# Kernel optimization log

Hardware: AMD Instinct MI355X
Metric: run time of the kernel (lower is better)

The kernel has to match this reference:

```python
import jax, jax.numpy as jnp
import numpy as np

IN_FEATURES = 1024
OUT_FEATURES = 1024
GRID_SIZE = 5
SPLINE_ORDER = 3
N_BASIS = GRID_SIZE + SPLINE_ORDER  # 8, matches spline_weight last dim
N_GRID = GRID_SIZE + 2 * SPLINE_ORDER + 1  # 12 knots -> Cox-de-Boor yields N_BASIS bases


def b_spline(x, grid):
    # x: [B, I] -> bases: [B, I, N_BASIS]
    x = x[..., None]
    bases = ((x >= grid[:-1]) & (x < grid[1:])).astype(x.dtype)
    for k in range(1, SPLINE_ORDER + 1):
        left = (x - grid[: -k - 1]) / (grid[k:-1] - grid[: -k - 1] + 1e-8)
        right = (grid[k + 1:] - x) / (grid[k + 1:] - grid[1:-k] + 1e-8)
        bases = left * bases[..., :-1] + right * bases[..., 1:]
    return bases


def setup_inputs() -> dict:
    key = jax.random.key(0)
    k1, k2, k3 = jax.random.split(key, 3)
    x = jax.random.uniform(k1, (4096, IN_FEATURES), dtype=jnp.float32) * 2.0 - 1.0
    # kaiming_uniform_(a=sqrt(5)) on [out,in]: bound = 1/sqrt(in)
    bound = 1.0 / np.sqrt(IN_FEATURES)
    base_weight = jax.random.uniform(k2, (OUT_FEATURES, IN_FEATURES), dtype=jnp.float32,
                                     minval=-bound, maxval=bound)
    spline_weight = 0.1 * jax.random.normal(k3, (OUT_FEATURES, IN_FEATURES, N_BASIS), dtype=jnp.float32)
    grid = jnp.linspace(-1.0, 1.0, N_GRID, dtype=jnp.float32)
    return {"x": x, "base_weight": base_weight, "spline_weight": spline_weight, "grid": grid}


def reference(x, base_weight, spline_weight, grid):
    base_output = jax.nn.silu(x) @ base_weight.T  # [B, O]
    spline_basis = b_spline(x, grid)              # [B, I, Q]
    spline_output = jnp.einsum('biq,oiq->bo', spline_basis, spline_weight)
    return base_output + spline_output
```

## Files before the change

kernel.cpp:

```cpp
#include <hip/hip_runtime.h>
#include <hip/hip_bf16.h>

#define IN_F 1024
#define OUT_F 1024
#define QP 9
#define KDIM (IN_F * QP)
#define BM 256
#define BN 256
#define BK 64
#define TILE_SH (BM * BK)

typedef __attribute__((ext_vector_type(8)))  short short8;
typedef __attribute__((ext_vector_type(16))) float floatx16;
typedef __attribute__((ext_vector_type(8)))  unsigned short ushort8v;

__device__ __forceinline__ unsigned short f2bf(float f) {
    union { float f; unsigned u; } v; v.f = f;
    return (unsigned short)((v.u + 0x7FFF + ((v.u >> 16) & 1)) >> 16);
}
__device__ __forceinline__ float bf2f(unsigned short h) {
    union { unsigned u; float f; } v; v.u = ((unsigned)h) << 16;
    return v.f;
}

__global__ __launch_bounds__(256) void pack_kernel(const float* __restrict__ x,
                                                   const float* __restrict__ bw,
                                                   const float* __restrict__ sw,
                                                   __hip_bfloat16* __restrict__ A,
                                                   __hip_bfloat16* __restrict__ W, int Bm) {
    const int nb_a = (Bm * IN_F / 8) / 256;
    if ((int)blockIdx.x < nb_a) {
        int t  = blockIdx.x * 256 + threadIdx.x;
        int b  = t >> 7;
        int i0 = (t & 127) * 8;
        const float4* xr = (const float4*)(x + (size_t)b * IN_F + i0);
        float4 x0 = xr[0], x1 = xr[1];
        float xv[8] = {x0.x, x0.y, x0.z, x0.w, x1.x, x1.y, x1.z, x1.w};
        ushort8v ov[9];
#pragma unroll
        for (int e = 0; e < 8; ++e) {
            float v  = xv[e];
            float u  = (v + 1.0f) * 5.5f;
            float fj = floorf(u);
            int   j  = (int)fj;
            float tt = u - fj;
            float t2 = tt * tt, t3 = t2 * tt;
            float omt = 1.0f - tt;
            float w0 = omt * omt * omt * (1.0f / 6.0f);
            float w1 = (3.0f * t3 - 6.0f * t2 + 4.0f) * (1.0f / 6.0f);
            float w2 = (-3.0f * t3 + 3.0f * t2 + 3.0f * tt + 1.0f) * (1.0f/6.0f);
            float w3 = t3 * (1.0f / 6.0f);
            ov[0][e] = f2bf(v * __builtin_amdgcn_rcpf(1.0f + __expf(-v)));
#pragma unroll
            for (int q = 0; q < 8; ++q) {
                int d = j - q;
                float bv = (d == 3) ? w0 : (d == 2) ? w1 : (d == 1) ? w2 : (d == 0) ? w3 : 0.0f;
                ov[1 + q][e] = f2bf(bv);
            }
        }
        unsigned short* dst = (unsigned short*)A + (size_t)b * KDIM + i0;
#pragma unroll
        for (int s = 0; s < QP; ++s)
            *(ushort8v*)(dst + (size_t)s * IN_F) = ov[s];
    } else {
        int t = ((int)blockIdx.x - nb_a) * 256 + threadIdx.x;
        unsigned short* dst = (unsigned short*)W + (size_t)(t >> 10) * KDIM + (t & 1023);
        dst[0] = f2bf(bw[t]);
        const float4* s4 = (const float4*)(sw + (size_t)t * 8);
        float4 lo = s4[0], hi = s4[1];
        dst[1 * IN_F] = f2bf(lo.x); dst[2 * IN_F] = f2bf(lo.y);
        dst[3 * IN_F] = f2bf(lo.z); dst[4 * IN_F] = f2bf(lo.w);
        dst[5 * IN_F] = f2bf(hi.x); dst[6 * IN_F] = f2bf(hi.y);
        dst[7 * IN_F] = f2bf(hi.z); dst[8 * IN_F] = f2bf(hi.w);
    }
}

#define GLD(src, dst) __builtin_amdgcn_global_load_lds( \
        (const __attribute__((address_space(1))) void*)(src), \
        (__attribute__((address_space(3))) void*)(dst), 16, 0, 0)

__global__ __launch_bounds__(512, 2) void gemm_splitk(const __hip_bfloat16* __restrict__ A,
                                                      const __hip_bfloat16* __restrict__ W,
                                                      unsigned short* __restrict__ P,
                                                      int Bm, int splitk, int kslice) {
    __shared__ __align__(16) short sA[2][TILE_SH];
    __shared__ __align__(16) short sB[2][TILE_SH];
    const int tid  = threadIdx.x;
    const int lane = tid & 63;
    const int wave = tid >> 6;
    const int r32  = lane & 31;
    const int half = lane >> 5;
    const int wm   = wave >> 2;
    const int wn   = wave & 3;

    const int b   = (int)blockIdx.x;
    const int xcd = b & 7, ii = b >> 3;
    const int pp  = xcd * (splitk >> 1) + (ii >> 4);
    const int xt  = pp & 3, zt = pp >> 2, yt = ii & 15;
    const int m0 = yt * BM, n0 = xt * BN, kb = zt * kslice;
    const int NT = kslice / BK;

    const short* Ag = (const short*)A + (size_t)m0 * KDIM + kb;
    const short* Wg = (const short*)W + (size_t)n0 * KDIM + kb;

    const short* pA[4]; const short* pB[4]; int ldst[4];
#pragma unroll
    for (int u = 0; u < 4; ++u) {
        int c  = u * 512 + tid;
        int gs = ((c & 7) ^ ((c >> 3) & 7)) * 8;
        pA[u] = Ag + (size_t)(c >> 3) * KDIM + gs;
        pB[u] = Wg + (size_t)(c >> 3) * KDIM + gs;
        ldst[u] = c * 8;
    }

    const int sw7 = r32 & 7;
    int offA[4][4], offB[2][4];
#pragma unroll
    for (int mi = 0; mi < 4; ++mi) {
        int row = wm * 128 + mi * 32 + r32;
#pragma unroll
        for (int kc = 0; kc < 4; ++kc)
            offA[mi][kc] = row * BK + (((kc * 2 + half) ^ sw7) * 8);
    }
#pragma unroll
    for (int ni = 0; ni < 2; ++ni) {
        int row = wn * 64 + ni * 32 + r32;
#pragma unroll
        for (int kc = 0; kc < 4; ++kc)
            offB[ni][kc] = row * BK + (((kc * 2 + half) ^ sw7) * 8);
    }

    floatx16 acc[4][2] = {};

#define STAGE(bi, koff) do { \
        _Pragma("unroll") \
        for (int u = 0; u < 4; ++u) { \
            GLD(pA[u] + (koff), &sA[bi][ldst[u]]); \
            GLD(pB[u] + (koff), &sB[bi][ldst[u]]); \
        } \
    } while (0)

    STAGE(0, 0);

    for (int t = 0; t < NT; ++t) {
        asm volatile("s_waitcnt vmcnt(0)" ::: "memory");
        __builtin_amdgcn_s_barrier();

        const int nb = (t + 1 == NT) ? 0 : t + 1;
        STAGE((t + 1) & 1, nb * BK);

        const short* sAb = &sA[t & 1][0];
        const short* sBb = &sB[t & 1][0];

        __builtin_amdgcn_s_setprio(1);
#pragma unroll
        for (int kc = 0; kc < 4; ++kc) {
            short8 aF[4], bF[2];
#pragma unroll
            for (int mi = 0; mi < 4; ++mi) aF[mi] = *(const short8*)(sAb + offA[mi][kc]);
#pragma unroll
            for (int ni = 0; ni < 2; ++ni) bF[ni] = *(const short8*)(sBb + offB[ni][kc]);
#pragma unroll
            for (int mi = 0; mi < 4; ++mi)
#pragma unroll
                for (int ni = 0; ni < 2; ++ni)
                    acc[mi][ni] = __builtin_amdgcn_mfma_f32_32x32x16_bf16(
                        aF[mi], bF[ni], acc[mi][ni], 0, 0, 0);
        }
        __builtin_amdgcn_s_setprio(0);
    }
#undef STAGE
    asm volatile("s_waitcnt vmcnt(0)" ::: "memory");

    unsigned short* Pz = P + (size_t)zt * Bm * OUT_F;
#pragma unroll
    for (int mi = 0; mi < 4; ++mi)
#pragma unroll
        for (int ni = 0; ni < 2; ++ni)
#pragma unroll
            for (int r = 0; r < 16; ++r) {
                int row = (r & 3) + 8 * (r >> 2) + 4 * half;
                int gm  = m0 + wm * 128 + mi * 32 + row;
                Pz[(size_t)gm * OUT_F + n0 + wn * 64 + ni * 32 + r32] = f2bf(acc[mi][ni][r]);
            }
}

__global__ __launch_bounds__(256) void reduce_kernel(const unsigned short* __restrict__ P,
                                                     float* __restrict__ C, int n, int s) {
    int t  = blockIdx.x * 256 + threadIdx.x;
    int i0 = t * 8;
    float o[8] = {0.f, 0.f, 0.f, 0.f, 0.f, 0.f, 0.f, 0.f};
    for (int j = 0; j < s; ++j) {
        ushort8v a = *(const ushort8v*)(P + (size_t)j * n + i0);
#pragma unroll
        for (int e = 0; e < 8; ++e) o[e] += bf2f(a[e]);
    }
    float4 o0, o1;
    o0.x = o[0]; o0.y = o[1]; o0.z = o[2]; o0.w = o[3];
    o1.x = o[4]; o1.y = o[5]; o1.z = o[6]; o1.w = o[7];
    *(float4*)(C + i0)     = o0;
    *(float4*)(C + i0 + 4) = o1;
}

__global__ __launch_bounds__(256) void fallback_kernel(const float* __restrict__ x,
                                                       const float* __restrict__ bw,
                                                       const float* __restrict__ sw,
                                                       const float* __restrict__ grid,
                                                       float* __restrict__ out, int Bm) {
    __shared__ float sv[256][QP + 1];
    int b = blockIdx.y;
    int o = blockIdx.x * 256 + threadIdx.x;
    float acc = 0.f;
    for (int ic = 0; ic < IN_F; ic += 256) {
        int i = ic + threadIdx.x;
        float v = x[(size_t)b * IN_F + i];
        float g[12];
        for (int j = 0; j < 12; ++j) g[j] = grid[j];
        float bb[11];
        for (int j = 0; j < 11; ++j) bb[j] = (v >= g[j] && v < g[j + 1]) ? 1.f : 0.f;
        for (int k = 1; k <= 3; ++k)
            for (int j = 0; j < 11 - k; ++j)
                bb[j] = (v - g[j]) / (g[j + k] - g[j] + 1e-8f) * bb[j]
                      + (g[j + k + 1] - v) / (g[j + k + 1] - g[j + 1] + 1e-8f) * bb[j + 1];
        __syncthreads();
        sv[threadIdx.x][0] = v / (1.f + __expf(-v));
        for (int q = 0; q < 8; ++q) sv[threadIdx.x][1 + q] = bb[q];
        __syncthreads();
        for (int ii = 0; ii < 256; ++ii) {
            int i2 = ic + ii;
            acc += sv[ii][0] * bw[(size_t)o * IN_F + i2];
            const float* swp = sw + ((size_t)o * IN_F + i2) * 8;
            for (int q = 0; q < 8; ++q) acc += sv[ii][1 + q] * swp[q];
        }
    }
    out[(size_t)b * OUT_F + o] = acc;
}

extern "C" void kernel_launch(void* const* d_in, const int* in_sizes, int n_in,
                              void* d_out, int out_size, void* d_ws, size_t ws_size,
                              hipStream_t stream) {
    const float* x    = (const float*)d_in[0];
    const float* bw   = (const float*)d_in[1];
    const float* sw   = (const float*)d_in[2];
    const float* grid = (const float*)d_in[3];
    float* out = (float*)d_out;

    const int Bm = in_sizes[0] / IN_F;
    const size_t a_bytes = (size_t)Bm * KDIM * sizeof(__hip_bfloat16);
    const size_t w_bytes = (size_t)OUT_F * KDIM * sizeof(__hip_bfloat16);

    int splitk = 4;
    size_t p_bytes = (size_t)splitk * Bm * OUT_F * sizeof(unsigned short);
    if (ws_size < a_bytes + w_bytes + p_bytes) {
        splitk = 2;
        p_bytes = (size_t)splitk * Bm * OUT_F * sizeof(unsigned short);
    }

    if (ws_size >= a_bytes + w_bytes + p_bytes && Bm == 4096) {
        __hip_bfloat16* Apk = (__hip_bfloat16*)d_ws;
        __hip_bfloat16* Wpk = (__hip_bfloat16*)((char*)d_ws + a_bytes);
        unsigned short* P = (unsigned short*)((char*)d_ws + a_bytes + w_bytes);
        const int nb_a = (Bm * IN_F / 8) / 256;
        const int nb_w = (OUT_F * IN_F) / 256;
        pack_kernel<<<nb_a + nb_w, 256, 0, stream>>>(x, bw, sw, Apk, Wpk, Bm);
        gemm_splitk<<<(Bm / BM) * (OUT_F / BN) * splitk, 512, 0, stream>>>(
            Apk, Wpk, P, Bm, splitk, KDIM / splitk);
        reduce_kernel<<<Bm * OUT_F / 2048, 256, 0, stream>>>(P, out, Bm * OUT_F, splitk);
    } else {
        fallback_kernel<<<dim3(OUT_F / 256, Bm), 256, 0, stream>>>(x, bw, sw, grid, out, Bm);
    }
}
```

Measured before the change: 197.5 us.

## Split K-tile into halves and interleave fine-grained staging with MFMA phases

Stores each K tile in LDS as two 32-wide halves with a new XOR swizzle. The main loop becomes eight phases per two K-tiles, and each phase issues a slice of the next tile's global-to-LDS loads between its fragment reads and its MFMAs. Waits drop from vmcnt(0) to partial vmcnt(4), so loads overlap compute rather than stalling once per tile. The cost is two barriers per phase instead of one per tile, and the loop assumes an even tile count.

```diff
diff --git a/kernel.cpp b/kernel.cpp
--- a/kernel.cpp
+++ b/kernel.cpp
@@ -8,7 +8,7 @@
 #define BM 256
 #define BN 256
 #define BK 64
-#define TILE_SH (BM * BK)
+#define KH_SH 8192
 
 typedef __attribute__((ext_vector_type(8)))  short short8;
 typedef __attribute__((ext_vector_type(16))) float floatx16;
@@ -79,12 +79,16 @@
         (const __attribute__((address_space(1))) void*)(src), \
         (__attribute__((address_space(3))) void*)(dst), 16, 0, 0)
 
+#define VM4 asm volatile("s_waitcnt vmcnt(4)" ::: "memory")
+#define VM0 asm volatile("s_waitcnt vmcnt(0)" ::: "memory")
+#define NOPW ((void)0)
+
 __global__ __launch_bounds__(512, 2) void gemm_splitk(const __hip_bfloat16* __restrict__ A,
                                                       const __hip_bfloat16* __restrict__ W,
                                                       unsigned short* __restrict__ P,
                                                       int Bm, int splitk, int kslice) {
-    __shared__ __align__(16) short sA[2][TILE_SH];
-    __shared__ __align__(16) short sB[2][TILE_SH];
+    __shared__ __align__(16) short sA[2][2 * KH_SH];
+    __shared__ __align__(16) short sB[2][2 * KH_SH];
     const int tid  = threadIdx.x;
     const int lane = tid & 63;
     const int wave = tid >> 6;
@@ -99,78 +103,87 @@
     const int xt  = pp & 3, zt = pp >> 2, yt = ii & 15;
     const int m0 = yt * BM, n0 = xt * BN, kb = zt * kslice;
     const int NT = kslice / BK;
+    const int NI = NT >> 1;
 
     const short* Ag = (const short*)A + (size_t)m0 * KDIM + kb;
     const short* Wg = (const short*)W + (size_t)n0 * KDIM + kb;
 
-    const short* pA[4]; const short* pB[4]; int ldst[4];
-#pragma unroll
-    for (int u = 0; u < 4; ++u) {
-        int c  = u * 512 + tid;
-        int gs = ((c & 7) ^ ((c >> 3) & 7)) * 8;
-        pA[u] = Ag + (size_t)(c >> 3) * KDIM + gs;
-        pB[u] = Wg + (size_t)(c >> 3) * KDIM + gs;
-        ldst[u] = c * 8;
-    }
-
-    const int sw7 = r32 & 7;
+    const int rc0 = tid >> 2, rc1 = rc0 + 128;
+    const int gw0 = (((tid & 3) ^ ((tid >> 3) & 3)) * 8);
+    const int ld0 = tid * 8, ld1 = ld0 + 4096;
+
+#define STG(S, Base, bi, Kh, k0) do { \
+        GLD(Base + (size_t)rc0 * KDIM + (k0) + (Kh) * 32 + gw0, &S[bi][(Kh) * KH_SH + ld0]); \
+        GLD(Base + (size_t)rc1 * KDIM + (k0) + (Kh) * 32 + gw0, &S[bi][(Kh) * KH_SH + ld1]); \
+    } while (0)
+
+    const int s2 = (r32 >> 1) & 3;
     int offA[4][4], offB[2][4];
 #pragma unroll
     for (int mi = 0; mi < 4; ++mi) {
         int row = wm * 128 + mi * 32 + r32;
 #pragma unroll
         for (int kc = 0; kc < 4; ++kc)
-            offA[mi][kc] = row * BK + (((kc * 2 + half) ^ sw7) * 8);
+            offA[mi][kc] = (kc >> 1) * KH_SH + row * 32 + ((((kc & 1) * 2 + half) ^ s2) * 8);
     }
 #pragma unroll
     for (int ni = 0; ni < 2; ++ni) {
         int row = wn * 64 + ni * 32 + r32;
 #pragma unroll
         for (int kc = 0; kc < 4; ++kc)
-            offB[ni][kc] = row * BK + (((kc * 2 + half) ^ sw7) * 8);
+            offB[ni][kc] = (kc >> 1) * KH_SH + row * 32 + ((((kc & 1) * 2 + half) ^ s2) * 8);
     }
 
     floatx16 acc[4][2] = {};
 
-#define STAGE(bi, koff) do { \
+#define PHASE(pb, kc, DO_STAGE, DO_WAIT) do { \
+        short8 aF[4], bF[2]; \
         _Pragma("unroll") \
-        for (int u = 0; u < 4; ++u) { \
-            GLD(pA[u] + (koff), &sA[bi][ldst[u]]); \
-            GLD(pB[u] + (koff), &sB[bi][ldst[u]]); \
-        } \
+        for (int mi = 0; mi < 4; ++mi) aF[mi] = *(const short8*)&sA[pb][offA[mi][kc]]; \
+        _Pragma("unroll") \
+        for (int ni = 0; ni < 2; ++ni) bF[ni] = *(const short8*)&sB[pb][offB[ni][kc]]; \
+        DO_STAGE; \
+        __builtin_amdgcn_s_barrier(); \
+        __builtin_amdgcn_s_setprio(1); \
+        _Pragma("unroll") \
+        for (int mi = 0; mi < 4; ++mi) \
+            _Pragma("unroll") \
+            for (int ni = 0; ni < 2; ++ni) \
+                acc[mi][ni] = __builtin_amdgcn_mfma_f32_32x32x16_bf16( \
+                    aF[mi], bF[ni], acc[mi][ni], 0, 0, 0); \
+        __builtin_amdgcn_s_setprio(0); \
+        DO_WAIT; \
+        __builtin_amdgcn_s_barrier(); \
     } while (0)
 
-    STAGE(0, 0);
-
-    for (int t = 0; t < NT; ++t) {
-        asm volatile("s_waitcnt vmcnt(0)" ::: "memory");
-        __builtin_amdgcn_s_barrier();
-
-        const int nb = (t + 1 == NT) ? 0 : t + 1;
-        STAGE((t + 1) & 1, nb * BK);
-
-        const short* sAb = &sA[t & 1][0];
-        const short* sBb = &sB[t & 1][0];
-
-        __builtin_amdgcn_s_setprio(1);
-#pragma unroll
-        for (int kc = 0; kc < 4; ++kc) {
-            short8 aF[4], bF[2];
-#pragma unroll
-            for (int mi = 0; mi < 4; ++mi) aF[mi] = *(const short8*)(sAb + offA[mi][kc]);
-#pragma unroll
-            for (int ni = 0; ni < 2; ++ni) bF[ni] = *(const short8*)(sBb + offB[ni][kc]);
-#pragma unroll
-            for (int mi = 0; mi < 4; ++mi)
-#pragma unroll
-                for (int ni = 0; ni < 2; ++ni)
-                    acc[mi][ni] = __builtin_amdgcn_mfma_f32_32x32x16_bf16(
-                        aF[mi], bF[ni], acc[mi][ni], 0, 0, 0);
+    STG(sA, Ag, 0, 0, 0);
+    STG(sB, Wg, 0, 0, 0);
+    STG(sA, Ag, 0, 1, 0);
+    STG(sB, Wg, 0, 1, 0);
+    VM4;
+    __builtin_amdgcn_s_barrier();
+
+    for (int it = 0; it < NI; ++it) {
+        const int k1 = (2 * it + 1) * BK;
+        const int k2 = (2 * it + 2) * BK;
+        PHASE(0, 0, STG(sA, Ag, 1, 0, k1), NOPW);
+        PHASE(0, 1, STG(sB, Wg, 1, 0, k1), VM4);
+        PHASE(0, 2, STG(sA, Ag, 1, 1, k1), NOPW);
+        PHASE(0, 3, STG(sB, Wg, 1, 1, k1), VM4);
+        if (it + 1 < NI) {
+            PHASE(1, 0, STG(sA, Ag, 0, 0, k2), NOPW);
+            PHASE(1, 1, STG(sB, Wg, 0, 0, k2), VM4);
+            PHASE(1, 2, STG(sA, Ag, 0, 1, k2), NOPW);
+            PHASE(1, 3, STG(sB, Wg, 0, 1, k2), VM4);
+        } else {
+            PHASE(1, 0, NOPW, NOPW);
+            PHASE(1, 1, NOPW, VM0);
+            PHASE(1, 2, NOPW, NOPW);
+            PHASE(1, 3, NOPW, NOPW);
         }
-        __builtin_amdgcn_s_setprio(0);
-    }
-#undef STAGE
-    asm volatile("s_waitcnt vmcnt(0)" ::: "memory");
+    }
+#undef PHASE
+#undef STG
 
     unsigned short* Pz = P + (size_t)zt * Bm * OUT_F;
 #pragma unroll
```

Result: slower. 294.5 us (+49.1%).

## Fuse split-K reduction into GEMM via per-tile atomic arrival counter

Applied to the files above, without the earlier changes.

Drops the separate reduce kernel. Each GEMM block writes its bf16 partial tile, bumps a per-output-tile atomic counter, and the last of the four split-K blocks to arrive sums the partials and writes the fp32 output. The pack kernel zeroes the counters. This saves one kernel launch and a full pass over the partial buffer by a separate grid, at the cost of fences, an atomic, and tail work done only by the last-arriving blocks. Split-K is now fixed at 4, so the fallback to split 2 when workspace is small is gone.

```diff
diff --git a/kernel.cpp b/kernel.cpp
--- a/kernel.cpp
+++ b/kernel.cpp
@@ -8,6 +8,7 @@
 #define BM 256
 #define BN 256
 #define BK 64
+#define SPLITK 4
 #define TILE_SH (BM * BK)
 
 typedef __attribute__((ext_vector_type(8)))  short short8;
@@ -27,7 +28,9 @@
                                                    const float* __restrict__ bw,
                                                    const float* __restrict__ sw,
                                                    __hip_bfloat16* __restrict__ A,
-                                                   __hip_bfloat16* __restrict__ W, int Bm) {
+                                                   __hip_bfloat16* __restrict__ W,
+                                                   int* __restrict__ cnt, int Bm) {
+    if (blockIdx.x == 0 && threadIdx.x < 64) cnt[threadIdx.x] = 0;
     const int nb_a = (Bm * IN_F / 8) / 256;
     if ((int)blockIdx.x < nb_a) {
         int t  = blockIdx.x * 256 + threadIdx.x;
@@ -82,9 +85,11 @@
 __global__ __launch_bounds__(512, 2) void gemm_splitk(const __hip_bfloat16* __restrict__ A,
                                                       const __hip_bfloat16* __restrict__ W,
                                                       unsigned short* __restrict__ P,
-                                                      int Bm, int splitk, int kslice) {
+                                                      float* __restrict__ out,
+                                                      int* __restrict__ cnt, int Bm) {
     __shared__ __align__(16) short sA[2][TILE_SH];
     __shared__ __align__(16) short sB[2][TILE_SH];
+    __shared__ int s_old;
     const int tid  = threadIdx.x;
     const int lane = tid & 63;
     const int wave = tid >> 6;
@@ -93,9 +98,10 @@
     const int wm   = wave >> 2;
     const int wn   = wave & 3;
 
+    const int kslice = KDIM / SPLITK;
     const int b   = (int)blockIdx.x;
     const int xcd = b & 7, ii = b >> 3;
-    const int pp  = xcd * (splitk >> 1) + (ii >> 4);
+    const int pp  = xcd * 2 + (ii >> 4);
     const int xt  = pp & 3, zt = pp >> 2, yt = ii & 15;
     const int m0 = yt * BM, n0 = xt * BN, kb = zt * kslice;
     const int NT = kslice / BK;
@@ -172,7 +178,8 @@
 #undef STAGE
     asm volatile("s_waitcnt vmcnt(0)" ::: "memory");
 
-    unsigned short* Pz = P + (size_t)zt * Bm * OUT_F;
+    const size_t bmout = (size_t)Bm * OUT_F;
+    unsigned short* Pz = P + (size_t)zt * bmout;
 #pragma unroll
     for (int mi = 0; mi < 4; ++mi)
 #pragma unroll
@@ -183,23 +190,36 @@
                 int gm  = m0 + wm * 128 + mi * 32 + row;
                 Pz[(size_t)gm * OUT_F + n0 + wn * 64 + ni * 32 + r32] = f2bf(acc[mi][ni][r]);
             }
-}
-
-__global__ __launch_bounds__(256) void reduce_kernel(const unsigned short* __restrict__ P,
-                                                     float* __restrict__ C, int n, int s) {
-    int t  = blockIdx.x * 256 + threadIdx.x;
-    int i0 = t * 8;
-    float o[8] = {0.f, 0.f, 0.f, 0.f, 0.f, 0.f, 0.f, 0.f};
-    for (int j = 0; j < s; ++j) {
-        ushort8v a = *(const ushort8v*)(P + (size_t)j * n + i0);
-#pragma unroll
-        for (int e = 0; e < 8; ++e) o[e] += bf2f(a[e]);
-    }
-    float4 o0, o1;
-    o0.x = o[0]; o0.y = o[1]; o0.z = o[2]; o0.w = o[3];
-    o1.x = o[4]; o1.y = o[5]; o1.z = o[6]; o1.w = o[7];
-    *(float4*)(C + i0)     = o0;
-    *(float4*)(C + i0 + 4) = o1;
+
+    __syncthreads();
+    __threadfence();
+    if (tid == 0)
+        s_old = __hip_atomic_fetch_add(&cnt[yt * 4 + xt], 1,
+                                       __ATOMIC_ACQ_REL, __HIP_MEMORY_SCOPE_AGENT);
+    __syncthreads();
+    if (s_old == 3) {
+        __threadfence();
+        const size_t base = (size_t)m0 * OUT_F + n0;
+#pragma unroll 2
+        for (int it2 = 0; it2 < 16; ++it2) {
+            int idx  = it2 * 512 + tid;
+            int row  = idx >> 5;
+            int colc = idx & 31;
+            size_t off = base + (size_t)row * OUT_F + colc * 8;
+            float o[8] = {0.f, 0.f, 0.f, 0.f, 0.f, 0.f, 0.f, 0.f};
+#pragma unroll
+            for (int z = 0; z < 4; ++z) {
+                ushort8v a8 = *(const ushort8v*)(P + (size_t)z * bmout + off);
+#pragma unroll
+                for (int e = 0; e < 8; ++e) o[e] += bf2f(a8[e]);
+            }
+            float4 o0, o1;
+            o0.x = o[0]; o0.y = o[1]; o0.z = o[2]; o0.w = o[3];
+            o1.x = o[4]; o1.y = o[5]; o1.z = o[6]; o1.w = o[7];
+            *(float4*)(out + off)     = o0;
+            *(float4*)(out + off + 4) = o1;
+        }
+    }
 }
 
 __global__ __launch_bounds__(256) void fallback_kernel(const float* __restrict__ x,
@@ -248,24 +268,19 @@
     const int Bm = in_sizes[0] / IN_F;
     const size_t a_bytes = (size_t)Bm * KDIM * sizeof(__hip_bfloat16);
     const size_t w_bytes = (size_t)OUT_F * KDIM * sizeof(__hip_bfloat16);
-
-    int splitk = 4;
-    size_t p_bytes = (size_t)splitk * Bm * OUT_F * sizeof(unsigned short);
-    if (ws_size < a_bytes + w_bytes + p_bytes) {
-        splitk = 2;
-        p_bytes = (size_t)splitk * Bm * OUT_F * sizeof(unsigned short);
-    }
-
-    if (ws_size >= a_bytes + w_bytes + p_bytes && Bm == 4096) {
+    const size_t p_bytes = (size_t)SPLITK * Bm * OUT_F * sizeof(unsigned short);
+    const size_t c_bytes = 256;
+
+    if (ws_size >= a_bytes + w_bytes + p_bytes + c_bytes && Bm == 4096) {
         __hip_bfloat16* Apk = (__hip_bfloat16*)d_ws;
         __hip_bfloat16* Wpk = (__hip_bfloat16*)((char*)d_ws + a_bytes);
         unsigned short* P = (unsigned short*)((char*)d_ws + a_bytes + w_bytes);
+        int* cnt = (int*)((char*)d_ws + a_bytes + w_bytes + p_bytes);
         const int nb_a = (Bm * IN_F / 8) / 256;
         const int nb_w = (OUT_F * IN_F) / 256;
-        pack_kernel<<<nb_a + nb_w, 256, 0, stream>>>(x, bw, sw, Apk, Wpk, Bm);
-        gemm_splitk<<<(Bm / BM) * (OUT_F / BN) * splitk, 512, 0, stream>>>(
-            Apk, Wpk, P, Bm, splitk, KDIM / splitk);
-        reduce_kernel<<<Bm * OUT_F / 2048, 256, 0, stream>>>(P, out, Bm * OUT_F, splitk);
+        pack_kernel<<<nb_a + nb_w, 256, 0, stream>>>(x, bw, sw, Apk, Wpk, cnt, Bm);
+        gemm_splitk<<<(Bm / BM) * (OUT_F / BN) * SPLITK, 512, 0, stream>>>(
+            Apk, Wpk, P, out, cnt, Bm);
     } else {
         fallback_kernel<<<dim3(OUT_F / 256, Bm), 256, 0, stream>>>(x, bw, sw, grid, out, Bm);
     }
```

Result: slower. 288.0 us (+45.8%).

## Shrink GEMM tile to 256x128 single-buffered for higher occupancy

Applied to the files above, without the earlier changes.

Reduces the split-K GEMM output tile from 256x256 to 256x128 and drops LDS double buffering in favour of a load-wait-compute-barrier loop. The aim is to fit more blocks per CU (launch bounds 6), so other resident blocks hide global-load latency. Split-K is fixed at compile time and the LDS swizzle is changed for the new tile shape. In exchange, each block reuses less data per loaded tile, global traffic for A doubles, and there is no longer any prefetch overlap within a block.

```diff
diff --git a/kernel.cpp b/kernel.cpp
--- a/kernel.cpp
+++ b/kernel.cpp
@@ -6,9 +6,11 @@
 #define QP 9
 #define KDIM (IN_F * QP)
 #define BM 256
-#define BN 256
+#define BN 128
 #define BK 64
-#define TILE_SH (BM * BK)
+#define SPLITK 4
+#define KSLICE (KDIM / SPLITK)
+#define NT (KSLICE / BK)
 
 typedef __attribute__((ext_vector_type(8)))  short short8;
 typedef __attribute__((ext_vector_type(16))) float floatx16;
@@ -79,118 +81,113 @@
         (const __attribute__((address_space(1))) void*)(src), \
         (__attribute__((address_space(3))) void*)(dst), 16, 0, 0)
 
-__global__ __launch_bounds__(512, 2) void gemm_splitk(const __hip_bfloat16* __restrict__ A,
+__global__ __launch_bounds__(512, 6) void gemm_splitk(const __hip_bfloat16* __restrict__ A,
                                                       const __hip_bfloat16* __restrict__ W,
-                                                      unsigned short* __restrict__ P,
-                                                      int Bm, int splitk, int kslice) {
-    __shared__ __align__(16) short sA[2][TILE_SH];
-    __shared__ __align__(16) short sB[2][TILE_SH];
+                                                      unsigned short* __restrict__ P, int Bm) {
+    __shared__ __align__(16) short sA[BM * BK];
+    __shared__ __align__(16) short sB[BN * BK];
     const int tid  = threadIdx.x;
     const int lane = tid & 63;
     const int wave = tid >> 6;
     const int r32  = lane & 31;
     const int half = lane >> 5;
-    const int wm   = wave >> 2;
-    const int wn   = wave & 3;
+    const int wm   = wave >> 1;
+    const int wn   = wave & 1;
 
     const int b   = (int)blockIdx.x;
     const int xcd = b & 7, ii = b >> 3;
-    const int pp  = xcd * (splitk >> 1) + (ii >> 4);
-    const int xt  = pp & 3, zt = pp >> 2, yt = ii & 15;
-    const int m0 = yt * BM, n0 = xt * BN, kb = zt * kslice;
-    const int NT = kslice / BK;
+    const int pp  = xcd * 4 + (ii >> 4);
+    const int xt  = pp & 7, zt = pp >> 3;
+    const int yt  = ii & 15;
+    const int m0 = yt * BM, n0 = xt * BN, kb = zt * KSLICE;
 
     const short* Ag = (const short*)A + (size_t)m0 * KDIM + kb;
     const short* Wg = (const short*)W + (size_t)n0 * KDIM + kb;
 
-    const short* pA[4]; const short* pB[4]; int ldst[4];
+    const short* pA[4]; const short* pB[2]; int ldA[4], ldB[2];
 #pragma unroll
     for (int u = 0; u < 4; ++u) {
         int c  = u * 512 + tid;
-        int gs = ((c & 7) ^ ((c >> 3) & 7)) * 8;
+        int gs = ((c & 7) ^ ((c >> 4) & 7)) * 8;
         pA[u] = Ag + (size_t)(c >> 3) * KDIM + gs;
+        ldA[u] = c * 8;
+    }
+#pragma unroll
+    for (int u = 0; u < 2; ++u) {
+        int c  = u * 512 + tid;
+        int gs = ((c & 7) ^ ((c >> 4) & 7)) * 8;
         pB[u] = Wg + (size_t)(c >> 3) * KDIM + gs;
-        ldst[u] = c * 8;
-    }
-
-    const int sw7 = r32 & 7;
-    int offA[4][4], offB[2][4];
-#pragma unroll
-    for (int mi = 0; mi < 4; ++mi) {
-        int row = wm * 128 + mi * 32 + r32;
+        ldB[u] = c * 8;
+    }
+
+    int offA[2][4], offB[2][4];
+#pragma unroll
+    for (int mi = 0; mi < 2; ++mi) {
+        int row = wm * 64 + mi * 32 + r32;
+        int sw  = (row >> 1) & 7;
 #pragma unroll
         for (int kc = 0; kc < 4; ++kc)
-            offA[mi][kc] = row * BK + (((kc * 2 + half) ^ sw7) * 8);
+            offA[mi][kc] = row * BK + (((kc * 2 + half) ^ sw) * 8);
     }
 #pragma unroll
     for (int ni = 0; ni < 2; ++ni) {
         int row = wn * 64 + ni * 32 + r32;
+        int sw  = (row >> 1) & 7;
 #pragma unroll
         for (int kc = 0; kc < 4; ++kc)
-            offB[ni][kc] = row * BK + (((kc * 2 + half) ^ sw7) * 8);
-    }
-
-    floatx16 acc[4][2] = {};
-
-#define STAGE(bi, koff) do { \
-        _Pragma("unroll") \
-        for (int u = 0; u < 4; ++u) { \
-            GLD(pA[u] + (koff), &sA[bi][ldst[u]]); \
-            GLD(pB[u] + (koff), &sB[bi][ldst[u]]); \
-        } \
-    } while (0)
-
-    STAGE(0, 0);
+            offB[ni][kc] = row * BK + (((kc * 2 + half) ^ sw) * 8);
+    }
+
+    floatx16 acc[2][2] = {};
 
     for (int t = 0; t < NT; ++t) {
+        const int koff = t * BK;
+#pragma unroll
+        for (int u = 0; u < 4; ++u) GLD(pA[u] + koff, &sA[ldA[u]]);
+#pragma unroll
+        for (int u = 0; u < 2; ++u) GLD(pB[u] + koff, &sB[ldB[u]]);
         asm volatile("s_waitcnt vmcnt(0)" ::: "memory");
         __builtin_amdgcn_s_barrier();
 
-        const int nb = (t + 1 == NT) ? 0 : t + 1;
-        STAGE((t + 1) & 1, nb * BK);
-
-        const short* sAb = &sA[t & 1][0];
-        const short* sBb = &sB[t & 1][0];
-
         __builtin_amdgcn_s_setprio(1);
 #pragma unroll
         for (int kc = 0; kc < 4; ++kc) {
-            short8 aF[4], bF[2];
-#pragma unroll
-            for (int mi = 0; mi < 4; ++mi) aF[mi] = *(const short8*)(sAb + offA[mi][kc]);
-#pragma unroll
-            for (int ni = 0; ni < 2; ++ni) bF[ni] = *(const short8*)(sBb + offB[ni][kc]);
-#pragma unroll
-            for (int mi = 0; mi < 4; ++mi)
+            short8 aF[2], bF[2];
+#pragma unroll
+            for (int mi = 0; mi < 2; ++mi) aF[mi] = *(const short8*)(sA + offA[mi][kc]);
+#pragma unroll
+            for (int ni = 0; ni < 2; ++ni) bF[ni] = *(const short8*)(sB + offB[ni][kc]);
+#pragma unroll
+            for (int mi = 0; mi < 2; ++mi)
 #pragma unroll
                 for (int ni = 0; ni < 2; ++ni)
                     acc[mi][ni] = __builtin_amdgcn_mfma_f32_32x32x16_bf16(
                         aF[mi], bF[ni], acc[mi][ni], 0, 0, 0);
         }
         __builtin_amdgcn_s_setprio(0);
-    }
-#undef STAGE
-    asm volatile("s_waitcnt vmcnt(0)" ::: "memory");
+        __builtin_amdgcn_s_barrier();
+    }
 
     unsigned short* Pz = P + (size_t)zt * Bm * OUT_F;
 #pragma unroll
-    for (int mi = 0; mi < 4; ++mi)
+    for (int mi = 0; mi < 2; ++mi)
 #pragma unroll
         for (int ni = 0; ni < 2; ++ni)
 #pragma unroll
             for (int r = 0; r < 16; ++r) {
                 int row = (r & 3) + 8 * (r >> 2) + 4 * half;
-                int gm  = m0 + wm * 128 + mi * 32 + row;
+                int gm  = m0 + wm * 64 + mi * 32 + row;
                 Pz[(size_t)gm * OUT_F + n0 + wn * 64 + ni * 32 + r32] = f2bf(acc[mi][ni][r]);
             }
 }
 
 __global__ __launch_bounds__(256) void reduce_kernel(const unsigned short* __restrict__ P,
-                                                     float* __restrict__ C, int n, int s) {
+                                                     float* __restrict__ C, int n) {
     int t  = blockIdx.x * 256 + threadIdx.x;
     int i0 = t * 8;
     float o[8] = {0.f, 0.f, 0.f, 0.f, 0.f, 0.f, 0.f, 0.f};
-    for (int j = 0; j < s; ++j) {
+#pragma unroll
+    for (int j = 0; j < SPLITK; ++j) {
         ushort8v a = *(const ushort8v*)(P + (size_t)j * n + i0);
 #pragma unroll
         for (int e = 0; e < 8; ++e) o[e] += bf2f(a[e]);
@@ -248,13 +245,7 @@
     const int Bm = in_sizes[0] / IN_F;
     const size_t a_bytes = (size_t)Bm * KDIM * sizeof(__hip_bfloat16);
     const size_t w_bytes = (size_t)OUT_F * KDIM * sizeof(__hip_bfloat16);
-
-    int splitk = 4;
-    size_t p_bytes = (size_t)splitk * Bm * OUT_F * sizeof(unsigned short);
-    if (ws_size < a_bytes + w_bytes + p_bytes) {
-        splitk = 2;
-        p_bytes = (size_t)splitk * Bm * OUT_F * sizeof(unsigned short);
-    }
+    const size_t p_bytes = (size_t)SPLITK * Bm * OUT_F * sizeof(unsigned short);
 
     if (ws_size >= a_bytes + w_bytes + p_bytes && Bm == 4096) {
         __hip_bfloat16* Apk = (__hip_bfloat16*)d_ws;
@@ -263,9 +254,8 @@
         const int nb_a = (Bm * IN_F / 8) / 256;
         const int nb_w = (OUT_F * IN_F) / 256;
         pack_kernel<<<nb_a + nb_w, 256, 0, stream>>>(x, bw, sw, Apk, Wpk, Bm);
-        gemm_splitk<<<(Bm / BM) * (OUT_F / BN) * splitk, 512, 0, stream>>>(
-            Apk, Wpk, P, Bm, splitk, KDIM / splitk);
-        reduce_kernel<<<Bm * OUT_F / 2048, 256, 0, stream>>>(P, out, Bm * OUT_F, splitk);
+        gemm_splitk<<<(Bm / BM) * (OUT_F / BN) * SPLITK, 512, 0, stream>>>(Apk, Wpk, P, Bm);
+        reduce_kernel<<<Bm * OUT_F / 2048, 256, 0, stream>>>(P, out, Bm * OUT_F);
     } else {
         fallback_kernel<<<dim3(OUT_F / 256, Bm), 256, 0, stream>>>(x, bw, sw, grid, out, Bm);
     }
```

Result: slower. 483.5 us (+144.8%).
